# Performance work log

Measured on AMD Instinct MI355X. Metric: run time of the kernel, lower is better.

Reference implementation:

```python
import jax, jax.numpy as jnp
import numpy as np
from jax import lax

H = 666
W = 666
EPS = 1e-5


def _conv(x, w, b):
    # NCHW conv, SAME padding, stride 1
    y = lax.conv_general_dilated(x, w, (1, 1), 'SAME',
                                 dimension_numbers=('NCHW', 'OIHW', 'NCHW'))
    return y + b[None, :, None, None]


def _bn2d(x, g, b):
    m = jnp.mean(x, (0, 2, 3), keepdims=True)
    v = jnp.var(x, (0, 2, 3), keepdims=True)
    return (x - m) * lax.rsqrt(v + EPS) * g[None, :, None, None] + b[None, :, None, None]


def _pool(x):
    return lax.reduce_window(x, -jnp.inf, lax.max, (1, 1, 2, 2), (1, 1, 2, 2), 'VALID')


def setup_inputs() -> dict:
    key = jax.random.key(0)
    ks = jax.random.split(key, 16)
    P, N, D = 20000, 32, 9

    def rn(k, shape, scale=0.05):
        return (jax.random.normal(k, shape, jnp.float32) * scale).astype(jnp.float32)

    return {
        'pillars': jax.random.normal(ks[0], (P, N, D), jnp.float32),
        'coords': jax.random.randint(ks[1], (P, 3), 0, 666, jnp.int64 if jax.config.jax_enable_x64 else jnp.int32),
        # PillarFeatureNet
        'lin_w': rn(ks[2], (64, 9)), 'lin_b': jnp.zeros((64,), jnp.float32),
        'pfn_g': jnp.ones((64,), jnp.float32), 'pfn_b': jnp.zeros((64,), jnp.float32),
        # Backbone
        'c1_w': rn(ks[3], (64, 64, 3, 3)), 'c1_b': jnp.zeros((64,), jnp.float32),
        'bn1_g': jnp.ones((64,), jnp.float32), 'bn1_b': jnp.zeros((64,), jnp.float32),
        'c2_w': rn(ks[4], (128, 64, 3, 3)), 'c2_b': jnp.zeros((128,), jnp.float32),
        'bn2_g': jnp.ones((128,), jnp.float32), 'bn2_b': jnp.zeros((128,), jnp.float32),
        # SSD head
        'h1_w': rn(ks[5], (256, 128, 3, 3)), 'h1_b': jnp.zeros((256,), jnp.float32),
        'hbn_g': jnp.ones((256,), jnp.float32), 'hbn_b': jnp.zeros((256,), jnp.float32),
        'hb_w': rn(ks[6], (21, 256, 3, 3)), 'hb_b': jnp.zeros((21,), jnp.float32),
        'hc_w': rn(ks[7], (3, 256, 3, 3)), 'hc_b': jnp.zeros((3,), jnp.float32),
    }


def reference(pillars, coords, lin_w, lin_b, pfn_g, pfn_b,
              c1_w, c1_b, bn1_g, bn1_b, c2_w, c2_b, bn2_g, bn2_b,
              h1_w, h1_b, hbn_g, hbn_b, hb_w, hb_b, hc_w, hc_b):
    P, N, D = pillars.shape
    # --- PillarFeatureNet: Linear -> BN1d (batch stats) -> ReLU -> max over points ---
    x = pillars.reshape(P * N, D) @ lin_w.T + lin_b           # [P*N, 64]
    m = jnp.mean(x, 0)
    v = jnp.var(x, 0)
    x = jax.nn.relu((x - m) * lax.rsqrt(v + EPS) * pfn_g + pfn_b)
    feats = jnp.max(x.reshape(P, N, -1), axis=1)              # [P, 64]

    # --- PseudoImageScatter: one vectorized scatter replacing the per-pillar loop ---
    y_idx = coords[:, 1]
    x_idx = coords[:, 2]
    valid = (y_idx >= 0) & (y_idx < H) & (x_idx >= 0) & (x_idx < W)
    y_idx = jnp.where(valid, y_idx, H)   # OOB -> dropped by scatter
    x_idx = jnp.where(valid, x_idx, W)
    img = jnp.zeros((64, H, W), feats.dtype).at[:, y_idx, x_idx].set(feats.T, mode='drop')
    img = img[None]                                           # [1, 64, H, W]

    # --- Backbone ---
    b1 = _pool(jax.nn.relu(_bn2d(_conv(img, c1_w, c1_b), bn1_g, bn1_b)))   # [1,64,333,333]
    b2 = _pool(jax.nn.relu(_bn2d(_conv(b1, c2_w, c2_b), bn2_g, bn2_b)))    # [1,128,166,166]

    # --- SSD head ---
    h = jax.nn.relu(_bn2d(_conv(b2, h1_w, h1_b), hbn_g, hbn_b))            # [1,256,166,166]
    bbox = _conv(h, hb_w, hb_b)                                            # [1,21,166,166]
    cls = _conv(h, hc_w, hc_b)                                             # [1,3,166,166]
    return (bbox, cls)
```

## Files before the change

kernel.cpp:

```cpp
#include <hip/hip_runtime.h>
#include <hip/hip_bf16.h>
#include <cstdint>
#include <cstddef>

#define BN_EPS 1e-5f

typedef short short8 __attribute__((ext_vector_type(8)));
typedef float float16 __attribute__((ext_vector_type(16)));
typedef unsigned short ushort_t;

__device__ __forceinline__ float bf2f(ushort_t u) {
  return __uint_as_float(((unsigned int)u) << 16);
}
__device__ __forceinline__ ushort_t f2bf(float f) {
  unsigned int u = __float_as_uint(f);
  u += 0x7FFFu + ((u >> 16) & 1u);
  return (ushort_t)(u >> 16);
}

__device__ __forceinline__ void gload16(const ushort_t* g, ushort_t* l) {
  __builtin_amdgcn_global_load_lds(
      (const __attribute__((address_space(1))) unsigned int*)g,
      (__attribute__((address_space(3))) unsigned int*)l, 16, 0, 0);
}


__global__ __launch_bounds__(512) void pillar_moments(
    const float* __restrict__ pillars, float* __restrict__ mom) {
  float S[9], M[45];
#pragma unroll
  for (int i = 0; i < 9; ++i) S[i] = 0.f;
#pragma unroll
  for (int i = 0; i < 45; ++i) M[i] = 0.f;
  const int t = blockIdx.x * 512 + threadIdx.x;
  const int NTH = 128 * 512;
  for (long r = t; r < 640000; r += NTH) {
    float x[9];
    const float* rp = pillars + r * 9;
#pragma unroll
    for (int d = 0; d < 9; ++d) x[d] = rp[d];
    int k = 0;
#pragma unroll
    for (int i = 0; i < 9; ++i) {
      S[i] += x[i];
#pragma unroll
      for (int j = i; j < 9; ++j) { M[k] += x[i] * x[j]; ++k; }
    }
  }
#pragma unroll
  for (int i = 0; i < 9; ++i)
#pragma unroll
    for (int o = 32; o > 0; o >>= 1) S[i] += __shfl_xor(S[i], o);
#pragma unroll
  for (int i = 0; i < 45; ++i)
#pragma unroll
    for (int o = 32; o > 0; o >>= 1) M[i] += __shfl_xor(M[i], o);
  __shared__ float red[8 * 54];
  int lane = threadIdx.x & 63, wv = threadIdx.x >> 6;
  if (lane == 0) {
#pragma unroll
    for (int i = 0; i < 9; ++i) red[wv * 54 + i] = S[i];
#pragma unroll
    for (int i = 0; i < 45; ++i) red[wv * 54 + 9 + i] = M[i];
  }
  __syncthreads();
  if (threadIdx.x < 54) {
    float s = 0.f;
#pragma unroll
    for (int w8 = 0; w8 < 8; ++w8) s += red[w8 * 54 + threadIdx.x];
    atomicAdd(&mom[threadIdx.x], s);
  }
}

__global__ void pfn_finalize(const float* __restrict__ mom,
                             const float* __restrict__ lin_w,
                             const float* __restrict__ lin_b,
                             const float* __restrict__ g, const float* __restrict__ b,
                             float* __restrict__ ss) {
  int c = threadIdx.x;
  double w[9], S[9];
#pragma unroll
  for (int d = 0; d < 9; ++d) {
    w[d] = (double)lin_w[c * 9 + d];
    S[d] = (double)mom[d];
  }
  double wS = 0.0;
#pragma unroll
  for (int d = 0; d < 9; ++d) wS += w[d] * S[d];
  double wMw = 0.0;
  int k = 0;
#pragma unroll
  for (int i = 0; i < 9; ++i)
#pragma unroll
    for (int j = i; j < 9; ++j) {
      double m = (double)mom[9 + k];
      wMw += (i == j ? 1.0 : 2.0) * w[i] * w[j] * m;
      ++k;
    }
  const double N = 640000.0;
  double bc = (double)lin_b[c];
  double mean = (wS + N * bc) / N;
  double ey2 = (wMw + 2.0 * bc * wS + N * bc * bc) / N;
  double var = ey2 - mean * mean;
  if (var < 0.0) var = 0.0;
  double inv = 1.0 / sqrt(var + (double)BN_EPS);
  double sc = (double)g[c] * inv;
  ss[c] = (float)sc;
  ss[c + 64] = (float)((double)b[c] - mean * sc);
}

__global__ __launch_bounds__(256) void pfn_feats(
    const float* __restrict__ pillars, const float* __restrict__ lin_w,
    const float* __restrict__ lin_b, const float* __restrict__ ss,
    ushort_t* __restrict__ feats) {
  __shared__ float s_p[1152];
  int tid = threadIdx.x;
  int c = tid & 63, pe = tid >> 6;
  long pb = (long)blockIdx.x * 4;
  for (int i = tid; i < 1152; i += 256) s_p[i] = pillars[pb * 288 + i];
  float w[9];
#pragma unroll
  for (int d = 0; d < 9; ++d) w[d] = lin_w[c * 9 + d];
  float bl = lin_b[c];
  float sc = ss[c], sh = ss[c + 64];
  __syncthreads();
  const float* pp = &s_p[pe * 288];
  float m = -1e30f;
#pragma unroll 4
  for (int n = 0; n < 32; ++n) {
    float y = bl;
#pragma unroll
    for (int d = 0; d < 9; ++d) y += pp[n * 9 + d] * w[d];
    float v = fmaxf(y * sc + sh, 0.f);
    m = fmaxf(m, v);
  }
  feats[(pb + pe) * 64 + c] = f2bf(m);
}


__global__ void scatter_winner(const int* __restrict__ coords, int* __restrict__ winner,
                               int P) {
  int p = blockIdx.x * 256 + threadIdx.x;
  if (p >= P) return;
  int y = coords[p * 3 + 1], x = coords[p * 3 + 2];
  if (y >= 0 && y < 666 && x >= 0 && x < 666) atomicMax(&winner[y * 666 + x], p);
}


__device__ __forceinline__ void prep_one(const float* __restrict__ w,
                                         ushort_t* __restrict__ w2, int C, int N,
                                         int Ntg, int chunks, int u) {
  int total = chunks * 9 * 2 * Ntg * 64;
  if (u >= total) return;
  int l = u & 63;
  int g = u >> 6;
  int ntg = g % Ntg;
  int g2 = g / Ntg;
  int s = g2 & 1;
  int g3 = g2 >> 1;
  int pos = g3 % 9;
  int cc = g3 / 9;
  int n = ntg * 32 + (l & 31);
  int c0 = cc * 32 + s * 16 + (l >> 5) * 8;
  ushort_t o8[8];
#pragma unroll
  for (int j = 0; j < 8; ++j) {
    int c = c0 + j;
    float v = (n < N && c < C) ? w[((size_t)n * C + c) * 9 + pos] : 0.f;
    o8[j] = f2bf(v);
  }
  *(uint4*)&w2[(size_t)u * 8] = *(const uint4*)o8;
}

__device__ __forceinline__ void prep_head_one(const float* __restrict__ hb,
                                              const float* __restrict__ hc,
                                              ushort_t* __restrict__ w2, int u) {
  int total = 8 * 9 * 2 * 64;
  if (u >= total) return;
  int l = u & 63;
  int g = u >> 6;
  int s = g & 1;
  int g3 = g >> 1;
  int pos = g3 % 9;
  int cc = g3 / 9;
  int n = l & 31;
  int c0 = cc * 32 + s * 16 + (l >> 5) * 8;
  ushort_t o8[8];
#pragma unroll
  for (int j = 0; j < 8; ++j) {
    int c = c0 + j;
    float v = 0.f;
    if (n < 21) v = hb[((size_t)n * 256 + c) * 9 + pos];
    else if (n < 24) v = hc[((size_t)(n - 21) * 256 + c) * 9 + pos];
    o8[j] = f2bf(v);
  }
  *(uint4*)&w2[(size_t)u * 8] = *(const uint4*)o8;
}

__global__ void prep_all(const float* __restrict__ c1_w, const float* __restrict__ c2_w,
                         const float* __restrict__ h1_w, const float* __restrict__ hb_w,
                         const float* __restrict__ hc_w, ushort_t* __restrict__ w2c1,
                         ushort_t* __restrict__ w2c2, ushort_t* __restrict__ w2h1,
                         ushort_t* __restrict__ w2hd) {
  int b = blockIdx.x;
  int t = threadIdx.x;
  if (b < 18) prep_one(c1_w, w2c1, 64, 64, 2, 2, b * 256 + t);
  else if (b < 54) prep_one(c2_w, w2c2, 64, 128, 4, 2, (b - 18) * 256 + t);
  else if (b < 198) prep_one(h1_w, w2h1, 128, 256, 8, 4, (b - 54) * 256 + t);
  else prep_head_one(hb_w, hc_w, w2hd, (b - 198) * 256 + t);
}


__global__ void bn_make_coefs(const float* __restrict__ acc, const float* __restrict__ g,
                              const float* __restrict__ b, float invN,
                              float* __restrict__ coef, int C) {
  int c = threadIdx.x;
  if (c >= C) return;
  float m = acc[c] * invN;
  float v = fmaxf(acc[c + 256] * invN - m * m, 0.f);
  float sc = g[c] * rsqrtf(v + BN_EPS);
  coef[c] = sc;
  coef[C + c] = b[c] - m * sc;
}


__global__ __launch_bounds__(256) void bnrelu(const ushort_t* __restrict__ inp,
                                              const float* __restrict__ coef, int C,
                                              int L8, ushort_t* __restrict__ outp) {
  __shared__ float sc[512];
  int tid = threadIdx.x;
  for (int i = tid; i < 2 * C; i += 256) sc[i] = coef[i];
  __syncthreads();
  int t = blockIdx.x * 256 + tid;
  if (t >= L8) return;
  size_t e0 = (size_t)t * 8;
  int c0 = (t << 3) & (C - 1);
  short8 v = *(const short8*)&inp[e0];
  const ushort_t* vp = (const ushort_t*)&v;
  ushort_t o[8];
#pragma unroll
  for (int j = 0; j < 8; ++j) {
    float x = bf2f(vp[j]);
    o[j] = f2bf(fmaxf(x * sc[c0 + j] + sc[C + c0 + j], 0.f));
  }
  *(uint4*)&outp[e0] = *(const uint4*)o;
}


template <int NT, int WAVES, bool GATHER, bool HEAD, bool STATS, bool POOL>
__global__ __launch_bounds__(WAVES * 64, 4) void conv_mfma(
    const ushort_t* __restrict__ in, const int* __restrict__ winner,
    const ushort_t* __restrict__ feats, const ushort_t* __restrict__ w2,
    const float* __restrict__ bias, const float* __restrict__ bias2,
    const ushort_t* __restrict__ zbuf, ushort_t* __restrict__ obf,
    float* __restrict__ hpart, float* __restrict__ statacc, int W, int H, int C,
    int nchunks, int Ntg) {
  constexpr int NTHREADS = WAVES * 64;
  constexpr int NPOS = (WAVES + 2) * 66;
  constexpr int IN_U4 = NPOS * 2;
  constexpr int W_U4 = 9 * NT * 64;
  constexpr int INIT = (IN_U4 + NTHREADS - 1) / NTHREADS;
  constexpr int WIT = (W_U4 + NTHREADS - 1) / NTHREADS;
  __shared__ ushort_t s_in[2][IN_U4 * 8];
  __shared__ ushort_t s_w[2][W_U4 * 8];
  const int tid = threadIdx.x;
  const int lane = tid & 63, wv = tid >> 6;
  const int lc = lane & 31, lh = lane >> 5;
  const int x0 = blockIdx.x * 64, y0 = blockIdx.y * WAVES;
  const int z = blockIdx.z;
  const int cc0 = HEAD ? z * nchunks : 0;
  const int z_oc = HEAD ? 0 : z;

  int pc[2][3];
#pragma unroll
  for (int Mt = 0; Mt < 2; ++Mt)
#pragma unroll
    for (int kx = 0; kx < 3; ++kx) {
      int col = Mt * 32 + kx + lc;
      pc[Mt][kx] = col * 16 + (lh ^ (col & 1)) * 8;
    }

  const ushort_t* isrc[INIT];
#pragma unroll
  for (int it = 0; it < INIT; ++it) {
    isrc[it] = zbuf;
    int d = it * NTHREADS + tid;
    if (d < IN_U4) {
      int p = d >> 1, g = d & 1;
      int r = p / 66, col = p - r * 66;
      int cg = g ^ (col & 1);
      int gy = y0 - 1 + r, gx = x0 - 1 + col;
      if (gy >= 0 && gy < H && gx >= 0 && gx < W) {
        if (GATHER) {
          int pw = winner[gy * 666 + gx];
          if (pw >= 0) isrc[it] = feats + pw * 64 + cg * 8;
        } else {
          isrc[it] = in + (size_t)(gy * W + gx) * C + cg * 8;
        }
      }
    }
  }
  int wof[WIT];
#pragma unroll
  for (int it = 0; it < WIT; ++it) {
    wof[it] = 0;
    int d = it * NTHREADS + tid;
    if (d < W_U4) {
      int grp = d >> 6, l16 = d & 63;
      int pos = grp / NT, nt = grp % NT;
      wof[it] = (pos * 2 * Ntg + z_oc * NT + nt) * 512 + l16 * 8;
    }
  }

  float bv[NT];
#pragma unroll
  for (int nt = 0; nt < NT; ++nt) {
    if (HEAD) {
      bv[nt] = (z == 0) ? (lc < 21 ? bias[lc] : (lc < 24 ? bias2[lc - 21] : 0.f)) : 0.f;
    } else {
      bv[nt] = bias[(z * NT + nt) * 32 + lc];
    }
  }
  float16 acc[2][NT];
#pragma unroll
  for (int Mt = 0; Mt < 2; ++Mt)
#pragma unroll
    for (int nt = 0; nt < NT; ++nt)
#pragma unroll
      for (int r = 0; r < 16; ++r) acc[Mt][nt][r] = bv[nt];

  auto stage = [&](int ph, int b) {
    int ccg = cc0 + (ph >> 1), sh = ph & 1;
    int coff = ccg * 32 + sh * 16;
#pragma unroll
    for (int it = 0; it < INIT; ++it) {
      int d = it * NTHREADS + tid;
      if (d < IN_U4)
        gload16(isrc[it] + coff, &s_in[b][(size_t)(it * NTHREADS + wv * 64) * 8]);
    }
    int wbase = (ccg * 18 + sh) * Ntg * 512;
#pragma unroll
    for (int it = 0; it < WIT; ++it) {
      int d = it * NTHREADS + tid;
      if (d < W_U4)
        gload16(w2 + wbase + wof[it], &s_w[b][(size_t)(it * NTHREADS + wv * 64) * 8]);
    }
  };

  auto compute_phase = [&](int b) {
#pragma unroll
    for (int ky = 0; ky < 3; ++ky) {
      const ushort_t* rowp = &s_in[b][(wv + ky) * (66 * 16)];
#pragma unroll
      for (int kx = 0; kx < 3; ++kx) {
        const int pos = ky * 3 + kx;
        short8 Bf[NT];
#pragma unroll
        for (int nt = 0; nt < NT; ++nt)
          Bf[nt] = *(const short8*)&s_w[b][(pos * NT + nt) * 512 + lane * 8];
#pragma unroll
        for (int Mt = 0; Mt < 2; ++Mt) {
          short8 Af = *(const short8*)&rowp[pc[Mt][kx]];
#pragma unroll
          for (int nt = 0; nt < NT; ++nt)
            acc[Mt][nt] =
                __builtin_amdgcn_mfma_f32_32x32x16_bf16(Af, Bf[nt], acc[Mt][nt], 0, 0, 0);
        }
      }
    }
  };

  const int nph = nchunks * 2;
  stage(0, 0);
  for (int ph = 0; ph < nph; ++ph) {
    asm volatile("s_waitcnt vmcnt(0)\n\ts_barrier" ::: "memory");
    if (ph + 1 < nph) stage(ph + 1, (ph + 1) & 1);
    __builtin_amdgcn_s_setprio(1);
    compute_phase(ph & 1);
    __builtin_amdgcn_s_setprio(0);
  }

  const int y = y0 + wv;
  const bool yok = (y < H);
  const int Ntot = Ntg * 32;

  if (HEAD) {
    if (yok) {
      float* hp = hpart + (size_t)z * (size_t)(H * W) * 32;
#pragma unroll
      for (int Mt = 0; Mt < 2; ++Mt)
#pragma unroll
        for (int r = 0; r < 16; ++r) {
          int m = (r & 3) + 8 * (r >> 2) + 4 * lh;
          int x = x0 + Mt * 32 + m;
          if (x < W) {
            size_t sp = (size_t)y * W + x;
            hp[sp * 32 + lc] = acc[Mt][0][r];
          }
        }
    }
    return;
  }

  if (!POOL) {
    if (yok) {
#pragma unroll
      for (int Mt = 0; Mt < 2; ++Mt)
#pragma unroll
        for (int r = 0; r < 16; ++r) {
          int m = (r & 3) + 8 * (r >> 2) + 4 * lh;
          int x = x0 + Mt * 32 + m;
          if (x < W) {
            size_t sp = (size_t)y * W + x;
#pragma unroll
            for (int nt = 0; nt < NT; ++nt) {
              int oc = (z * NT + nt) * 32 + lc;
              obf[sp * Ntot + oc] = f2bf(acc[Mt][nt][r]);
            }
          }
        }
    }
  }

  if (STATS) {
    float s1[NT], s2[NT];
#pragma unroll
    for (int nt = 0; nt < NT; ++nt) { s1[nt] = 0.f; s2[nt] = 0.f; }
    if (yok) {
#pragma unroll
      for (int Mt = 0; Mt < 2; ++Mt)
#pragma unroll
        for (int r = 0; r < 16; ++r) {
          int m = (r & 3) + 8 * (r >> 2) + 4 * lh;
          int x = x0 + Mt * 32 + m;
          if (x < W) {
#pragma unroll
            for (int nt = 0; nt < NT; ++nt) {
              float v = acc[Mt][nt][r];
              s1[nt] += v;
              s2[nt] += v * v;
            }
          }
        }
    }
#pragma unroll
    for (int nt = 0; nt < NT; ++nt) {
      s1[nt] += __shfl_xor(s1[nt], 32);
      s2[nt] += __shfl_xor(s2[nt], 32);
    }
    __syncthreads();
    float* red = (float*)s_in;
    if (lh == 0) {
#pragma unroll
      for (int nt = 0; nt < NT; ++nt) {
        red[(wv * NT + nt) * 32 + lc] = s1[nt];
        red[WAVES * NT * 32 + (wv * NT + nt) * 32 + lc] = s2[nt];
      }
    }
    __syncthreads();
    if (wv == 0 && lh == 0) {
#pragma unroll
      for (int nt = 0; nt < NT; ++nt) {
        float a = 0.f, b = 0.f;
#pragma unroll
        for (int w8 = 0; w8 < WAVES; ++w8) {
          a += red[(w8 * NT + nt) * 32 + lc];
          b += red[WAVES * NT * 32 + (w8 * NT + nt) * 32 + lc];
        }
        int ch = (z * NT + nt) * 32 + lc;
        atomicAdd(&statacc[ch], a);
        atomicAdd(&statacc[ch + 256], b);
      }
    }
  }

  if (POOL) {
    const int OWp = W >> 1, OHp = H >> 1;
    float hm[2][NT][8];
#pragma unroll
    for (int Mt = 0; Mt < 2; ++Mt)
#pragma unroll
      for (int nt = 0; nt < NT; ++nt)
#pragma unroll
        for (int i = 0; i < 8; ++i)
          hm[Mt][nt][i] = fmaxf(acc[Mt][nt][2 * i], acc[Mt][nt][2 * i + 1]);
    __syncthreads();
    float* pl = (float*)s_in;
    if (wv & 1) {
#pragma unroll
      for (int Mt = 0; Mt < 2; ++Mt)
#pragma unroll
        for (int nt = 0; nt < NT; ++nt)
#pragma unroll
          for (int i = 0; i < 8; ++i)
            pl[((((wv >> 1) * 2 + Mt) * NT + nt) * 8 + i) * 64 + lane] = hm[Mt][nt][i];
    }
    __syncthreads();
    if (!(wv & 1)) {
      int oy = (y0 + wv) >> 1;
      if (oy < OHp) {
#pragma unroll
        for (int Mt = 0; Mt < 2; ++Mt)
#pragma unroll
          for (int i = 0; i < 8; ++i) {
            int pxl = Mt * 16 + (i >> 1) * 4 + (i & 1) + 2 * lh;
            int ox = (x0 >> 1) + pxl;
            if (ox < OWp) {
#pragma unroll
              for (int nt = 0; nt < NT; ++nt) {
                float v = fmaxf(
                    hm[Mt][nt][i],
                    pl[((((wv >> 1) * 2 + Mt) * NT + nt) * 8 + i) * 64 + lane]);
                int oc = (z * NT + nt) * 32 + lc;
                obf[((size_t)oy * OWp + ox) * Ntot + oc] = f2bf(v);
              }
            }
          }
      }
    }
  }
}


__global__ __launch_bounds__(256) void head_reduce(const float* __restrict__ hp,
                                                   float* __restrict__ out, int HW,
                                                   int nz) {
  __shared__ float t[256 * 33];
  int tid = threadIdx.x;
  int sp0 = blockIdx.x * 256;
  int lim = (HW - sp0) * 32;
#pragma unroll 4
  for (int i = 0; i < 32; ++i) {
    int e = i * 256 + tid;
    float s = 0.f;
    if (e < lim) {
      size_t gidx = (size_t)sp0 * 32 + e;
      for (int z = 0; z < nz; ++z) s += hp[(size_t)z * HW * 32 + gidx];
    }
    t[(e >> 5) * 33 + (e & 31)] = s;
  }
  __syncthreads();
  int sp = sp0 + tid;
  if (sp < HW) {
#pragma unroll
    for (int ch = 0; ch < 24; ++ch)
      out[(size_t)ch * HW + sp] = t[tid * 33 + ch];
  }
}


extern "C" void kernel_launch(void* const* d_in, const int* in_sizes, int n_in,
                              void* d_out, int out_size, void* d_ws, size_t ws_size,
                              hipStream_t stream) {
  (void)in_sizes; (void)n_in; (void)out_size; (void)ws_size;
  const float* pillars = (const float*)d_in[0];
  const int* coords = (const int*)d_in[1];
  const float* lin_w = (const float*)d_in[2];
  const float* lin_b = (const float*)d_in[3];
  const float* pfn_g = (const float*)d_in[4];
  const float* pfn_b = (const float*)d_in[5];
  const float* c1_w = (const float*)d_in[6];
  const float* c1_b = (const float*)d_in[7];
  const float* bn1_g = (const float*)d_in[8];
  const float* bn1_b = (const float*)d_in[9];
  const float* c2_w = (const float*)d_in[10];
  const float* c2_b = (const float*)d_in[11];
  const float* bn2_g = (const float*)d_in[12];
  const float* bn2_b = (const float*)d_in[13];
  const float* h1_w = (const float*)d_in[14];
  const float* h1_b = (const float*)d_in[15];
  const float* hbn_g = (const float*)d_in[16];
  const float* hbn_b = (const float*)d_in[17];
  const float* hb_w = (const float*)d_in[18];
  const float* hb_b = (const float*)d_in[19];
  const float* hc_w = (const float*)d_in[20];
  const float* hc_b = (const float*)d_in[21];
  float* out = (float*)d_out;

  char* ws = (char*)d_ws;
  float* mom     = (float*)(ws + 0);
  float* pfn_ss  = (float*)(ws + 512);
  float* bn_acc1 = (float*)(ws + 1024);
  float* bn_acc2 = (float*)(ws + 3072);
  float* bn_acc3 = (float*)(ws + 5120);
  float* coef1   = (float*)(ws + 7168);
  float* coef2   = (float*)(ws + 7680);
  float* coef3   = (float*)(ws + 8704);
  ushort_t* zbuf = (ushort_t*)(ws + 10752);
  int* winner    = (int*)(ws + 11264);
  ushort_t* feats  = (ushort_t*)(ws + 1785600);
  ushort_t* c1p    = (ushort_t*)(ws + 4345600);
  ushort_t* c2a    = (ushort_t*)(ws + 4345600);
  ushort_t* c2p    = (ushort_t*)(ws + 18539392);
  ushort_t* h1out  = (ushort_t*)(ws + 25593728);
  ushort_t* w2c1   = (ushort_t*)(ws + 39702400);
  ushort_t* w2c2   = (ushort_t*)(ws + 39776128);
  ushort_t* w2h1   = (ushort_t*)(ws + 39923584);
  ushort_t* w2hd   = (ushort_t*)(ws + 40513408);
  float* hpart     = (float*)(ws + 40660864);
  ushort_t* c1a    = (ushort_t*)(ws + 54769536);
  ushort_t* h1a    = (ushort_t*)(ws + 54769536);

  const int HW3 = 166 * 166;

  hipMemsetAsync(ws, 0, 11264, stream);
  hipMemsetAsync(winner, 0xFF, 1774224, stream);

  prep_all<<<234, 256, 0, stream>>>(c1_w, c2_w, h1_w, hb_w, hc_w, w2c1, w2c2, w2h1,
                                    w2hd);

  pillar_moments<<<128, 512, 0, stream>>>(pillars, mom);
  pfn_finalize<<<1, 64, 0, stream>>>(mom, lin_w, lin_b, pfn_g, pfn_b, pfn_ss);
  pfn_feats<<<5000, 256, 0, stream>>>(pillars, lin_w, lin_b, pfn_ss, feats);

  scatter_winner<<<(20000 + 255) / 256, 256, 0, stream>>>(coords, winner, 20000);

  conv_mfma<2, 8, true, false, true, true><<<dim3(11, 84, 1), 512, 0, stream>>>(
      nullptr, winner, feats, w2c1, c1_b, nullptr, zbuf, c1p, nullptr, bn_acc1, 666,
      666, 64, 2, 2);
  bn_make_coefs<<<1, 64, 0, stream>>>(bn_acc1, bn1_g, bn1_b, 1.f / 443556.f, coef1, 64);

  bnrelu<<<(887112 + 255) / 256, 256, 0, stream>>>(c1p, coef1, 64, 887112, c1a);

  conv_mfma<2, 8, false, false, true, true><<<dim3(6, 42, 2), 512, 0, stream>>>(
      c1a, nullptr, nullptr, w2c2, c2_b, nullptr, zbuf, c2p, nullptr, bn_acc2, 333, 333,
      64, 2, 4);
  bn_make_coefs<<<1, 128, 0, stream>>>(bn_acc2, bn2_g, bn2_b, 1.f / 110889.f, coef2, 128);

  bnrelu<<<(440896 + 255) / 256, 256, 0, stream>>>(c2p, coef2, 128, 440896, c2a);

  conv_mfma<2, 4, false, false, true, false><<<dim3(3, 42, 4), 256, 0, stream>>>(
      c2a, nullptr, nullptr, w2h1, h1_b, nullptr, zbuf, h1out, nullptr, bn_acc3, 166,
      166, 128, 4, 8);
  bn_make_coefs<<<1, 256, 0, stream>>>(bn_acc3, hbn_g, hbn_b, 1.f / 27556.f, coef3, 256);

  bnrelu<<<(881792 + 255) / 256, 256, 0, stream>>>(h1out, coef3, 256, 881792, h1a);

  conv_mfma<1, 4, false, true, false, false><<<dim3(3, 42, 4), 256, 0, stream>>>(
      h1a, nullptr, nullptr, w2hd, hb_b, hc_b, zbuf, nullptr, hpart, nullptr, 166,
      166, 256, 2, 1);
  head_reduce<<<(HW3 + 255) / 256, 256, 0, stream>>>(hpart, out, HW3, 4);
}
```

Measured before the change: 323.0 us.

## Triple-buffer conv MFMA LDS staging with partial vmcnt waits

Replaces the double-buffered global-to-LDS staging in the conv kernel with a three-stage ring. Two phases are prefetched ahead, and each step uses partial s_waitcnt vmcnt counts instead of draining all loads. Out-of-range load lanes now write to a junk LDS buffer instead of being predicated off, so the per-wave load count is uniform and the vmcnt counting stays valid. The launch-bounds occupancy hint drops from 4 to 2 to make room for the larger LDS footprint, and the head convs switch to 8-wave blocks. This trades occupancy and LDS size for deeper latency hiding, and it relies on the hardcoded vmcnt values matching the number of loads issued per stage.

Result: slower. 338.3 us (+4.7%).

```diff
diff --git a/kernel.cpp b/kernel.cpp
--- a/kernel.cpp
+++ b/kernel.cpp
@@ -248,7 +248,7 @@
 
 
 template <int NT, int WAVES, bool GATHER, bool HEAD, bool STATS, bool POOL>
-__global__ __launch_bounds__(WAVES * 64, 4) void conv_mfma(
+__global__ __launch_bounds__(WAVES * 64, 2) void conv_mfma(
     const ushort_t* __restrict__ in, const int* __restrict__ winner,
     const ushort_t* __restrict__ feats, const ushort_t* __restrict__ w2,
     const float* __restrict__ bias, const float* __restrict__ bias2,
@@ -261,8 +261,11 @@
   constexpr int W_U4 = 9 * NT * 64;
   constexpr int INIT = (IN_U4 + NTHREADS - 1) / NTHREADS;
   constexpr int WIT = (W_U4 + NTHREADS - 1) / NTHREADS;
-  __shared__ ushort_t s_in[2][IN_U4 * 8];
-  __shared__ ushort_t s_w[2][W_U4 * 8];
+  constexpr int NL = INIT + WIT;
+  constexpr int IN_SLOTS = ((IN_U4 + 63) / 64) * 64;
+  __shared__ ushort_t s_in[3][IN_SLOTS * 8];
+  __shared__ ushort_t s_w[3][W_U4 * 8];
+  __shared__ ushort_t s_junk[512];
   const int tid = threadIdx.x;
   const int lane = tid & 63, wv = tid >> 6;
   const int lc = lane & 31, lh = lane >> 5;
@@ -330,20 +333,20 @@
       for (int r = 0; r < 16; ++r) acc[Mt][nt][r] = bv[nt];
 
   auto stage = [&](int ph, int b) {
-    int ccg = cc0 + (ph >> 1), sh = ph & 1;
-    int coff = ccg * 32 + sh * 16;
+    const int ccg = cc0 + (ph >> 1), sh2 = ph & 1;
+    const int coff = ccg * 32 + sh2 * 16;
 #pragma unroll
     for (int it = 0; it < INIT; ++it) {
-      int d = it * NTHREADS + tid;
-      if (d < IN_U4)
-        gload16(isrc[it] + coff, &s_in[b][(size_t)(it * NTHREADS + wv * 64) * 8]);
-    }
-    int wbase = (ccg * 18 + sh) * Ntg * 512;
+      int span = it * NTHREADS + wv * 64;
+      ushort_t* dst = (span < IN_SLOTS) ? &s_in[b][(size_t)span * 8] : s_junk;
+      gload16(isrc[it] + coff, dst);
+    }
+    const int wbase = (ccg * 18 + sh2) * Ntg * 512;
 #pragma unroll
     for (int it = 0; it < WIT; ++it) {
-      int d = it * NTHREADS + tid;
-      if (d < W_U4)
-        gload16(w2 + wbase + wof[it], &s_w[b][(size_t)(it * NTHREADS + wv * 64) * 8]);
+      int span = it * NTHREADS + wv * 64;
+      ushort_t* dst = (span < W_U4) ? &s_w[b][(size_t)span * 8] : s_junk;
+      gload16(w2 + wbase + wof[it], dst);
     }
   };
 
@@ -371,12 +374,22 @@
   };
 
   const int nph = nchunks * 2;
+  asm volatile("s_waitcnt vmcnt(0)" ::: "memory");
   stage(0, 0);
+  stage(1, 1);
   for (int ph = 0; ph < nph; ++ph) {
-    asm volatile("s_waitcnt vmcnt(0)\n\ts_barrier" ::: "memory");
-    if (ph + 1 < nph) stage(ph + 1, (ph + 1) & 1);
+    if (ph + 1 < nph) {
+      if constexpr (NL == 6) asm volatile("s_waitcnt vmcnt(6)" ::: "memory");
+      else if constexpr (NL == 5) asm volatile("s_waitcnt vmcnt(5)" ::: "memory");
+      else if constexpr (NL == 4) asm volatile("s_waitcnt vmcnt(4)" ::: "memory");
+      else asm volatile("s_waitcnt vmcnt(0)" ::: "memory");
+    } else {
+      asm volatile("s_waitcnt vmcnt(0)" ::: "memory");
+    }
+    asm volatile("s_barrier" ::: "memory");
+    if (ph + 2 < nph) stage(ph + 2, (ph + 2) % 3);
     __builtin_amdgcn_s_setprio(1);
-    compute_phase(ph & 1);
+    compute_phase(ph % 3);
     __builtin_amdgcn_s_setprio(0);
   }
 
@@ -629,14 +642,14 @@
 
   bnrelu<<<(440896 + 255) / 256, 256, 0, stream>>>(c2p, coef2, 128, 440896, c2a);
 
-  conv_mfma<2, 4, false, false, true, false><<<dim3(3, 42, 4), 256, 0, stream>>>(
+  conv_mfma<2, 8, false, false, true, false><<<dim3(3, 21, 4), 512, 0, stream>>>(
       c2a, nullptr, nullptr, w2h1, h1_b, nullptr, zbuf, h1out, nullptr, bn_acc3, 166,
       166, 128, 4, 8);
   bn_make_coefs<<<1, 256, 0, stream>>>(bn_acc3, hbn_g, hbn_b, 1.f / 27556.f, coef3, 256);
 
   bnrelu<<<(881792 + 255) / 256, 256, 0, stream>>>(h1out, coef3, 256, 881792, h1a);
 
-  conv_mfma<1, 4, false, true, false, false><<<dim3(3, 42, 4), 256, 0, stream>>>(
+  conv_mfma<1, 8, false, true, false, false><<<dim3(3, 21, 4), 512, 0, stream>>>(
       h1a, nullptr, nullptr, w2hd, hb_b, hc_b, zbuf, nullptr, hpart, nullptr, 166,
       166, 256, 2, 1);
   head_reduce<<<(HW3 + 255) / 256, 256, 0, stream>>>(hpart, out, HW3, 4);
```
